# Optimization experiments

Measured on AMD Instinct MI355X. Metric: run time of the kernel, lower is better.

## Reference

```python
import jax, jax.numpy as jnp
import numpy as np

B, H, W, C = 4, 64, 64, 96
EXPAND = 2
D_INNER = EXPAND * C  # 192
N = 16   # d_state
K = 4    # scan directions
DT_RANK = int(np.ceil(C / 16))  # 6


def setup_inputs() -> dict:
    key = jax.random.key(0)
    ks = jax.random.split(key, 8)
    def rn(k, shape, scale=0.02):
        return jax.random.normal(k, shape, dtype=jnp.float32) * scale
    return {
        "x": jax.random.normal(ks[0], (B, H, W, C), dtype=jnp.float32),
        "ln_g": jnp.ones((C,), jnp.float32),
        "ln_b": jnp.zeros((C,), jnp.float32),
        "in_proj_w": rn(ks[1], (C, 2 * D_INNER)),
        "in_proj_b": jnp.zeros((2 * D_INNER,), jnp.float32),
        "conv_w": rn(ks[2], (D_INNER, 1, 3, 3), 0.1),
        "conv_b": jnp.zeros((D_INNER,), jnp.float32),
        "x_proj_w": rn(ks[3], (K, DT_RANK + 2 * N, D_INNER)),
        "dt_proj_w": rn(ks[4], (K, D_INNER, DT_RANK), 0.1),
        "dt_proj_b": rn(ks[5], (K, D_INNER), 0.1),
        "A_logs": jnp.log(jnp.tile(jnp.arange(1, N + 1, dtype=jnp.float32)[None, :], (K * D_INNER, 1))),
        "Ds": jnp.ones((K * D_INNER,), jnp.float32),
        "out_norm_g": jnp.ones((D_INNER,), jnp.float32),
        "out_norm_b": jnp.zeros((D_INNER,), jnp.float32),
        "out_proj_w": rn(ks[6], (D_INNER, C)),
        "out_proj_b": jnp.zeros((C,), jnp.float32),
    }


def _ln(x, g, b, eps):
    mu = x.mean(-1, keepdims=True)
    var = jnp.mean((x - mu) ** 2, axis=-1, keepdims=True)
    return (x - mu) * jax.lax.rsqrt(var + eps) * g + b


def _vss_forward(x, ln_g, ln_b, in_proj_w, in_proj_b, conv_w, conv_b,
                 x_proj_w, dt_proj_w, dt_proj_b, A_logs, Ds,
                 out_norm_g, out_norm_b, out_proj_w, out_proj_b):
    Bb, Hh, Ww, Cc = x.shape
    L = Hh * Ww
    d = D_INNER
    # ln_1 (eps=1e-6), then SS2D on channels-first layout
    xn = _ln(x, ln_g, ln_b, 1e-6)
    xz = jnp.einsum('bhwc,ce->bhwe', xn, in_proj_w) + in_proj_b
    xi, z = jnp.split(xz, 2, axis=-1)
    xi = xi.transpose(0, 3, 1, 2)  # (B, d, H, W)
    xi = jax.lax.conv_general_dilated(
        xi, conv_w, (1, 1), 'SAME', feature_group_count=d,
        dimension_numbers=('NCHW', 'OIHW', 'NCHW'))
    xi = jax.nn.silu(xi + conv_b[None, :, None, None])
    # 4 scan directions: row-major, col-major, and their reverses
    x_hw = xi.reshape(Bb, d, L)
    x_wh = xi.transpose(0, 1, 3, 2).reshape(Bb, d, L)
    xs = jnp.stack([x_hw, x_wh], axis=1)                      # (B,2,d,L)
    xs = jnp.concatenate([xs, jnp.flip(xs, axis=-1)], axis=1)  # (B,K,d,L)
    x_dbl = jnp.einsum('bkdl,kcd->bkcl', xs, x_proj_w)         # (B,K,R+2N,L)
    dt_r = x_dbl[:, :, :DT_RANK]
    Bs = x_dbl[:, :, DT_RANK:DT_RANK + N]                      # (B,K,N,L)
    Cs = x_dbl[:, :, DT_RANK + N:]                             # (B,K,N,L)
    dts = jnp.einsum('bkrl,kdr->bkdl', dt_r, dt_proj_w)
    dts = jax.nn.softplus(dts + dt_proj_b[None, :, :, None])
    A = -jnp.exp(A_logs).reshape(K, d, N)
    Dsk = Ds.reshape(K, d)

    def step(h, inp):
        u_t, dt_t, B_t, C_t = inp                  # (B,K,d),(B,K,d),(B,K,N),(B,K,N)
        dA = jnp.exp(dt_t[..., None] * A)          # (B,K,d,N)
        h = dA * h + (dt_t * u_t)[..., None] * B_t[:, :, None, :]
        y = jnp.einsum('bkdn,bkn->bkd', h, C_t)
        return h, y

    seq = (xs.transpose(3, 0, 1, 2), dts.transpose(3, 0, 1, 2),
           Bs.transpose(3, 0, 1, 2), Cs.transpose(3, 0, 1, 2))
    h0 = jnp.zeros((Bb, K, d, N), xs.dtype)
    _, ys = jax.lax.scan(step, h0, seq)            # ys: (L,B,K,d)
    ys = ys.transpose(1, 2, 3, 0)                  # (B,K,d,L)
    ys = ys + Dsk[None, :, :, None] * xs
    # merge the 4 directions back into one row-major map
    inv_y = jnp.flip(ys[:, 2:4], axis=-1)
    wh_y = ys[:, 1].reshape(Bb, d, Ww, Hh).transpose(0, 1, 3, 2).reshape(Bb, d, L)
    invwh_y = inv_y[:, 1].reshape(Bb, d, Ww, Hh).transpose(0, 1, 3, 2).reshape(Bb, d, L)
    y = ys[:, 0] + inv_y[:, 0] + wh_y + invwh_y    # (B,d,L)
    y = y.transpose(0, 2, 1).reshape(Bb, Hh, Ww, d)
    y = _ln(y, out_norm_g, out_norm_b, 1e-5)
    y = y * jax.nn.silu(z)
    out = jnp.einsum('bhwd,dc->bhwc', y, out_proj_w) + out_proj_b
    return x + out  # residual (drop_path = 0 -> identity)


def reference(x, ln_g, ln_b, in_proj_w, in_proj_b, conv_w, conv_b, x_proj_w,
              dt_proj_w, dt_proj_b, A_logs, Ds, out_norm_g, out_norm_b,
              out_proj_w, out_proj_b):
    return _vss_forward(x, ln_g, ln_b, in_proj_w, in_proj_b, conv_w, conv_b,
                        x_proj_w, dt_proj_w, dt_proj_b, A_logs, Ds,
                        out_norm_g, out_norm_b, out_proj_w, out_proj_b)
```

## Files before the change

kernel.cpp:

```cpp
#include <hip/hip_runtime.h>
#include <math.h>

#define CC   96
#define DIN  192
#define NST  16
#define KDIR 4
#define DTR  6
#define LL   4096
#define BB   4
#define NSEG 64
#define SEGLEN 64
#define XROW 40

#define NROW ((long)BB*LL)
#define SZ_BLD ((long)BB*LL*DIN)

__device__ __forceinline__ float sigmoidf_(float x){
    return __builtin_amdgcn_rcpf(1.0f + __expf(-x));
}
__device__ __forceinline__ int whmap(int l){ return ((l & 63) << 6) | (l >> 6); }
__device__ __forceinline__ int mapk(int k, int l){
    switch(k & 3){
        case 0:  return l;
        case 1:  return whmap(l);
        case 2:  return LL - 1 - l;
        default: return whmap(LL - 1 - l);
    }
}

__global__ __launch_bounds__(384) void kA(const float* __restrict__ x,
        const float* __restrict__ lng, const float* __restrict__ lnb,
        const float* __restrict__ W,   const float* __restrict__ bias,
        float* __restrict__ xi, float* __restrict__ z)
{
    __shared__ float xn[16*96];
    __shared__ float sc1[384], sc2[384];
    __shared__ float mu[16], rs[16];
    int t = threadIdx.x;
    long row0 = (long)blockIdx.x * 16;

    for(int q=t; q<16*96; q+=384) xn[q] = x[row0*96 + q];
    __syncthreads();

    {
        int r = t/24, i = t%24;
        float s=0.f, ss=0.f;
        #pragma unroll
        for(int j=0;j<4;j++){ float v = xn[r*96 + i + j*24]; s+=v; ss+=v*v; }
        sc1[t]=s; sc2[t]=ss;
        __syncthreads();
        if(t<16){
            float S=0.f, SS=0.f;
            for(int j=0;j<24;j++){ S+=sc1[t*24+j]; SS+=sc2[t*24+j]; }
            float m = S*(1.0f/96.0f);
            float var = SS*(1.0f/96.0f) - m*m;
            mu[t]=m; rs[t]=rsqrtf(var + 1e-6f);
        }
        __syncthreads();
    }
    for(int q=t; q<16*96; q+=384){
        int r=q/96, c=q%96;
        xn[q] = (xn[q]-mu[r])*rs[r]*lng[c] + lnb[c];
    }
    __syncthreads();

    float acc[16];
    #pragma unroll
    for(int r=0;r<16;r++) acc[r]=0.f;
    for(int c=0;c<96;c++){
        float wv = W[c*384 + t];
        #pragma unroll
        for(int r=0;r<16;r++) acc[r] = fmaf(xn[r*96+c], wv, acc[r]);
    }
    float bv = bias[t];
    if(t < 192){
        for(int r=0;r<16;r++) xi[(row0+r)*DIN + t] = acc[r] + bv;
    } else {
        int e = t - 192;
        for(int r=0;r<16;r++) z[(row0+r)*DIN + e] = acc[r] + bv;
    }
}

__global__ __launch_bounds__(256) void kB(const float* __restrict__ xi,
        const float* __restrict__ cw, const float* __restrict__ cb,
        float* __restrict__ xc)
{
    long idx = (long)blockIdx.x*256 + threadIdx.x;
    if(idx >= SZ_BLD) return;
    int d = (int)(idx % DIN);
    long rg = idx / DIN;
    int p = (int)(rg % LL); int b = (int)(rg / LL);
    int h = p >> 6, w = p & 63;
    float acc = 0.f;
    #pragma unroll
    for(int dh=0; dh<3; dh++){
        int hh = h + dh - 1;
        if(hh < 0 || hh >= 64) continue;
        #pragma unroll
        for(int dw=0; dw<3; dw++){
            int ww2 = w + dw - 1;
            if(ww2 < 0 || ww2 >= 64) continue;
            acc = fmaf(xi[((long)b*LL + hh*64 + ww2)*DIN + d], cw[d*9 + dh*3 + dw], acc);
        }
    }
    acc += cb[d];
    xc[idx] = acc * sigmoidf_(acc);
}

__global__ __launch_bounds__(192) void kC(const float* __restrict__ xc,
        const float* __restrict__ xw, float* __restrict__ xdbl)
{
    __shared__ float ls[16*192];
    int t = threadIdx.x;
    long row0 = (long)blockIdx.x * 16;
    int b  = (int)(row0 / LL);
    int p0 = (int)(row0 % LL);
    for(int q=t; q<16*192; q+=192) ls[q] = xc[row0*DIN + q];
    __syncthreads();
    if(t < 152){
        int k = t/38, c = t%38;
        const float* wr = xw + (long)(k*38 + c)*192;
        float acc[16];
        #pragma unroll
        for(int r=0;r<16;r++) acc[r]=0.f;
        for(int d=0; d<192; d+=4){
            float4 wv = *(const float4*)(wr + d);
            #pragma unroll
            for(int r=0;r<16;r++){
                float4 lv = *(const float4*)(&ls[r*192 + d]);
                acc[r] = fmaf(lv.x,wv.x, fmaf(lv.y,wv.y, fmaf(lv.z,wv.z, fmaf(lv.w,wv.w, acc[r]))));
            }
        }
        int cs = (c < 6) ? c : c + 2;
        for(int r=0;r<16;r++){
            int p = p0 + r;
            int lk;
            if(k==0) lk = p;
            else if(k==1) lk = whmap(p);
            else if(k==2) lk = LL-1-p;
            else lk = LL-1-whmap(p);
            xdbl[(((long)(b*KDIR + k)*LL + lk)*XROW) + cs] = acc[r];
        }
    }
}

__device__ __forceinline__ void dt_and_E(float s, float& dt, float& E){
    float eneg = __expf(-fabsf(s));
    dt = fmaxf(s, 0.f) + log1pf(eneg);
    float rcp = __builtin_amdgcn_rcpf(1.0f + eneg);
    E = (s > 0.f) ? eneg*rcp : rcp;
}
__device__ __forceinline__ void pow_tree(float E, float* En){
    En[0]=E;
    float E2=E*E;        En[1]=E2;
    En[2]=E2*E;  float E4=E2*E2; En[3]=E4;
    En[4]=E4*E;  En[5]=E4*E2;  En[6]=E4*En[2];
    float E8=E4*E4;      En[7]=E8;
    En[8]=E8*E;  En[9]=E8*E2;  En[10]=E8*En[2]; En[11]=E8*E4;
    En[12]=E8*En[4]; En[13]=E8*En[5]; En[14]=E8*En[6]; En[15]=E8*E8;
}

__global__ __launch_bounds__(192) void kD(const float* __restrict__ xc,
        const float* __restrict__ xdbl, const float* __restrict__ alog,
        const float* __restrict__ dtw,  const float* __restrict__ dtb,
        const float* __restrict__ Ds,
        float* __restrict__ ys0, float* __restrict__ ys123,
        float* __restrict__ hend, float* __restrict__ dtsum)
{
    __shared__ float rows[SEGLEN*XROW];
    int t = threadIdx.x;
    int blk = blockIdx.x;
    int bk = blk / NSEG, seg = blk % NSEG;
    int b = bk / KDIR, k = bk % KDIR;
    {
        const float* src = xdbl + ((long)bk*LL + seg*SEGLEN)*XROW;
        for(int q=t; q<SEGLEN*XROW; q+=192) rows[q] = src[q];
    }
    int d = t;
    int kd = k*192 + d;
    float a[16]; bool fast = true;
    #pragma unroll
    for(int n=0;n<16;n++){
        a[n] = -__expf(alog[kd*16 + n]);
        fast = fast && (fabsf(a[n] + (float)(n+1)) < 1e-3f);
    }
    float w6[6];
    #pragma unroll
    for(int r=0;r<6;r++) w6[r] = dtw[kd*6 + r];
    float bdt = dtb[kd];
    float Dd  = Ds[kd];
    float* ybuf = (k==0) ? ys0 : (ys123 + (long)(k-1)*SZ_BLD);
    float h[16];
    #pragma unroll
    for(int n=0;n<16;n++) h[n]=0.f;
    float sdt = 0.f;
    __syncthreads();

    int lg0 = seg * SEGLEN;
    int p = mapk(k, lg0);
    float u = xc[((long)b*LL + p)*DIN + d];
    for(int i=0; i<SEGLEN; i++){
        const float* row = &rows[i*XROW];
        float s = bdt;
        #pragma unroll
        for(int r=0;r<6;r++) s = fmaf(row[r], w6[r], s);
        float dt, E; dt_and_E(s, dt, E);
        sdt += dt;
        float wi = dt * u;
        int pn = 0; float unext = 0.f;
        if(i+1 < SEGLEN){
            pn = mapk(k, lg0 + i + 1);
            unext = xc[((long)b*LL + pn)*DIN + d];
        }
        float En[16];
        if(fast){ pow_tree(E, En); }
        else { 
            #pragma unroll
            for(int n=0;n<16;n++) En[n] = __expf(dt * a[n]);
        }
        float Bv[16], Cv[16];
        #pragma unroll
        for(int n=0;n<16;n+=4){
            *(float4*)(Bv+n) = *(const float4*)(row + 8 + n);
            *(float4*)(Cv+n) = *(const float4*)(row + 24 + n);
        }
        float y = Dd * u;
        #pragma unroll
        for(int n=0;n<16;n++){
            h[n] = fmaf(En[n], h[n], wi*Bv[n]);
            y = fmaf(h[n], Cv[n], y);
        }
        ybuf[((long)b*LL + p)*DIN + d] = y;
        p = pn; u = unext;
    }
    long hb = (((long)bk*NSEG + seg)*192 + d)*16;
    #pragma unroll
    for(int n=0;n<16;n+=4)
        *(float4*)(&hend[hb+n]) = make_float4(h[n],h[n+1],h[n+2],h[n+3]);
    dtsum[((long)bk*NSEG + seg)*192 + d] = sdt;
}

__global__ __launch_bounds__(256) void kE(const float* __restrict__ alog,
        const float* __restrict__ dtsum, float* __restrict__ hx)
{
    int tid = blockIdx.x*256 + threadIdx.x;
    int n = tid & 15;
    int d = (tid >> 4) % 192;
    int bk = tid / (192*16);
    int k = bk % KDIR;
    float an = -__expf(alog[(k*192 + d)*16 + n]);
    float H = 0.f;
    for(int seg=0; seg<NSEG; seg++){
        long base = ((long)bk*NSEG + seg)*3072 + d*16 + n;
        float he = hx[base];
        hx[base] = H;
        float P = __expf(an * dtsum[((long)bk*NSEG + seg)*192 + d]);
        H = fmaf(P, H, he);
    }
}

__global__ __launch_bounds__(192) void kF(const float* __restrict__ xdbl,
        const float* __restrict__ alog, const float* __restrict__ dtw,
        const float* __restrict__ dtb,  const float* __restrict__ Hprev,
        float* __restrict__ ys0, float* __restrict__ ys123)
{
    int blk = blockIdx.x;
    int bk = blk / NSEG, seg = blk % NSEG;
    if(seg == 0) return;
    __shared__ float rows[SEGLEN*XROW];
    int t = threadIdx.x;
    int b = bk / KDIR, k = bk % KDIR;
    {
        const float* src = xdbl + ((long)bk*LL + seg*SEGLEN)*XROW;
        for(int q=t; q<SEGLEN*XROW; q+=192) rows[q] = src[q];
    }
    int d = t;
    int kd = k*192 + d;
    float a[16]; bool fast = true;
    #pragma unroll
    for(int n=0;n<16;n++){
        a[n] = -__expf(alog[kd*16 + n]);
        fast = fast && (fabsf(a[n] + (float)(n+1)) < 1e-3f);
    }
    float w6[6];
    #pragma unroll
    for(int r=0;r<6;r++) w6[r] = dtw[kd*6 + r];
    float bdt = dtb[kd];
    float g[16];
    long hb = (((long)bk*NSEG + seg)*192 + d)*16;
    #pragma unroll
    for(int n=0;n<16;n+=4){
        float4 v = *(const float4*)(&Hprev[hb+n]);
        g[n]=v.x; g[n+1]=v.y; g[n+2]=v.z; g[n+3]=v.w;
    }
    float* ybuf = (k==0) ? ys0 : (ys123 + (long)(k-1)*SZ_BLD);
    __syncthreads();

    int lg0 = seg * SEGLEN;
    int p = mapk(k, lg0);
    for(int i=0; i<SEGLEN; i++){
        const float* row = &rows[i*XROW];
        float s = bdt;
        #pragma unroll
        for(int r=0;r<6;r++) s = fmaf(row[r], w6[r], s);
        float dt, E; dt_and_E(s, dt, E);
        float En[16];
        if(fast){ pow_tree(E, En); }
        else {
            #pragma unroll
            for(int n=0;n<16;n++) En[n] = __expf(dt * a[n]);
        }
        float Cv[16];
        #pragma unroll
        for(int n=0;n<16;n+=4) *(float4*)(Cv+n) = *(const float4*)(row + 24 + n);
        float yc = 0.f;
        #pragma unroll
        for(int n=0;n<16;n++){
            g[n] *= En[n];
            yc = fmaf(g[n], Cv[n], yc);
        }
        long addr = ((long)b*LL + p)*DIN + d;
        ybuf[addr] += yc;
        if(i+1 < SEGLEN) p = mapk(k, lg0 + i + 1);
    }
}

__global__ __launch_bounds__(384) void kG(const float* __restrict__ ys0,
        const float* __restrict__ ys123, const float* __restrict__ z,
        const float* __restrict__ ong, const float* __restrict__ onb,
        const float* __restrict__ Wout, const float* __restrict__ ob,
        const float* __restrict__ x, float* __restrict__ out)
{
    __shared__ float yb[16*192];
    __shared__ float sc1[384], sc2[384];
    __shared__ float mu[16], rs[16];
    int t = threadIdx.x;
    long row0 = (long)blockIdx.x * 16;

    for(int q=t; q<3072; q+=384){
        long off = row0*DIN + q;
        yb[q] = ys0[off] + ys123[off] + ys123[SZ_BLD + off] + ys123[2*SZ_BLD + off];
    }
    __syncthreads();
    {
        int r = t/24, i = t%24;
        float s=0.f, ss=0.f;
        #pragma unroll
        for(int j=0;j<8;j++){ float v = yb[r*192 + i*8 + j]; s+=v; ss+=v*v; }
        sc1[t]=s; sc2[t]=ss;
        __syncthreads();
        if(t<16){
            float S=0.f, SS=0.f;
            for(int j=0;j<24;j++){ S+=sc1[t*24+j]; SS+=sc2[t*24+j]; }
            float m = S*(1.0f/192.0f);
            float var = SS*(1.0f/192.0f) - m*m;
            mu[t]=m; rs[t]=rsqrtf(var + 1e-5f);
        }
        __syncthreads();
    }
    for(int q=t; q<3072; q+=384){
        int r=q/192, dd=q%192;
        float v = (yb[q]-mu[r])*rs[r]*ong[dd] + onb[dd];
        float zz = z[row0*DIN + q];
        yb[q] = v * (zz * sigmoidf_(zz));
    }
    __syncthreads();
    int c = t % 96, rg4 = t / 96;
    float acc[4] = {0.f,0.f,0.f,0.f};
    for(int dd=0; dd<192; dd++){
        float wv = Wout[dd*96 + c];
        #pragma unroll
        for(int j=0;j<4;j++) acc[j] = fmaf(yb[(rg4*4+j)*192 + dd], wv, acc[j]);
    }
    float bv = ob[c];
    for(int j=0;j<4;j++){
        long row = row0 + rg4*4 + j;
        out[row*96 + c] = x[row*96 + c] + acc[j] + bv;
    }
}

extern "C" void kernel_launch(void* const* d_in, const int* in_sizes, int n_in,
                              void* d_out, int out_size, void* d_ws, size_t ws_size,
                              hipStream_t stream)
{
    const float* x    = (const float*)d_in[0];
    const float* lng  = (const float*)d_in[1];
    const float* lnb  = (const float*)d_in[2];
    const float* ipw  = (const float*)d_in[3];
    const float* ipb  = (const float*)d_in[4];
    const float* cw   = (const float*)d_in[5];
    const float* cb   = (const float*)d_in[6];
    const float* xpw  = (const float*)d_in[7];
    const float* dtw  = (const float*)d_in[8];
    const float* dtb  = (const float*)d_in[9];
    const float* alog = (const float*)d_in[10];
    const float* Ds   = (const float*)d_in[11];
    const float* ong  = (const float*)d_in[12];
    const float* onb  = (const float*)d_in[13];
    const float* opw  = (const float*)d_in[14];
    const float* opb  = (const float*)d_in[15];

    float* ws    = (float*)d_ws;
    float* xi    = ws + 0;
    float* z     = ws + 3145728;
    float* xc    = ws + 6291456;
    float* xdbl  = ws + 9437184;
    float* ys123 = ws + 12058624;
    float* hx    = ws + 21495808;
    float* dtsum = ws + 24641536;
    float* ys0   = xi;
    float* out   = (float*)d_out;

    hipLaunchKernelGGL(kA, dim3(1024),  dim3(384), 0, stream, x, lng, lnb, ipw, ipb, xi, z);
    hipLaunchKernelGGL(kB, dim3(12288), dim3(256), 0, stream, xi, cw, cb, xc);
    hipLaunchKernelGGL(kC, dim3(1024),  dim3(192), 0, stream, xc, xpw, xdbl);
    hipLaunchKernelGGL(kD, dim3(1024),  dim3(192), 0, stream, xc, xdbl, alog, dtw, dtb, Ds,
                       ys0, ys123, hx, dtsum);
    hipLaunchKernelGGL(kE, dim3(192),   dim3(256), 0, stream, alog, dtsum, hx);
    hipLaunchKernelGGL(kF, dim3(1024),  dim3(192), 0, stream, xdbl, alog, dtw, dtb, hx,
                       ys0, ys123);
    hipLaunchKernelGGL(kG, dim3(1024),  dim3(384), 0, stream, ys0, ys123, z, ong, onb,
                       opw, opb, x, out);
}
```

Measured before the change: 343.1 us.

## Restructure chunked scan: state-only first pass, full recompute with carry-in second pass

The first scan pass now computes only the per-segment end states and dt sums, without producing outputs. The second pass starts from the propagated carry-in state and recomputes the full recurrence, so it writes final y directly instead of doing a read-modify-write correction. Segment length is halved to double the number of blocks. The carry-propagation kernel is reorganized to one block per (batch, direction) with prefetching, and softplus/exp use exp2/log intrinsics with strided address stepping. The cost is recomputing the recurrence in the second pass and the kE2 pass now being serial over 128 segments in only 16 blocks.

```diff
diff --git a/kernel.cpp b/kernel.cpp
--- a/kernel.cpp
+++ b/kernel.cpp
@@ -8,11 +8,10 @@
 #define DTR  6
 #define LL   4096
 #define BB   4
-#define NSEG 64
-#define SEGLEN 64
+#define NSEG 128
+#define SEGLEN 32
 #define XROW 40
 
-#define NROW ((long)BB*LL)
 #define SZ_BLD ((long)BB*LL*DIN)
 
 __device__ __forceinline__ float sigmoidf_(float x){
@@ -28,6 +27,34 @@
     }
 }
 
+__device__ __forceinline__ void dt_and_E(float s, float& dt, float& E){
+    const float LOG2E = 1.4426950408889634f;
+    const float LN2   = 0.6931471805599453f;
+    float sn  = s * LOG2E;
+    float t   = __builtin_amdgcn_exp2f(-fabsf(sn));
+    float opt = 1.0f + t;
+    float r   = __builtin_amdgcn_rcpf(opt);
+    E  = (s > 0.f) ? t*r : r;
+    dt = LN2 * (fmaxf(sn, 0.f) + __builtin_amdgcn_logf(opt));
+}
+__device__ __forceinline__ void pow_tree(float E, float* En){
+    En[0]=E;
+    float E2=E*E;        En[1]=E2;
+    En[2]=E2*E;  float E4=E2*E2; En[3]=E4;
+    En[4]=E4*E;  En[5]=E4*E2;  En[6]=E4*En[2];
+    float E8=E4*E4;      En[7]=E8;
+    En[8]=E8*E;  En[9]=E8*E2;  En[10]=E8*En[2]; En[11]=E8*E4;
+    En[12]=E8*En[4]; En[13]=E8*En[5]; En[14]=E8*En[6]; En[15]=E8*E8;
+}
+__device__ __forceinline__ void dir_base(int k, int lg0, int& p0, int& stride){
+    switch(k & 3){
+        case 0:  p0 = lg0;               stride = 1;   break;
+        case 1:  p0 = whmap(lg0);        stride = 64;  break;
+        case 2:  p0 = LL - 1 - lg0;      stride = -1;  break;
+        default: p0 = whmap(LL-1-lg0);   stride = -64; break;
+    }
+}
+
 __global__ __launch_bounds__(384) void kA(const float* __restrict__ x,
         const float* __restrict__ lng, const float* __restrict__ lnb,
         const float* __restrict__ W,   const float* __restrict__ bias,
@@ -41,7 +68,6 @@
 
     for(int q=t; q<16*96; q+=384) xn[q] = x[row0*96 + q];
     __syncthreads();
-
     {
         int r = t/24, i = t%24;
         float s=0.f, ss=0.f;
@@ -144,27 +170,9 @@
     }
 }
 
-__device__ __forceinline__ void dt_and_E(float s, float& dt, float& E){
-    float eneg = __expf(-fabsf(s));
-    dt = fmaxf(s, 0.f) + log1pf(eneg);
-    float rcp = __builtin_amdgcn_rcpf(1.0f + eneg);
-    E = (s > 0.f) ? eneg*rcp : rcp;
-}
-__device__ __forceinline__ void pow_tree(float E, float* En){
-    En[0]=E;
-    float E2=E*E;        En[1]=E2;
-    En[2]=E2*E;  float E4=E2*E2; En[3]=E4;
-    En[4]=E4*E;  En[5]=E4*E2;  En[6]=E4*En[2];
-    float E8=E4*E4;      En[7]=E8;
-    En[8]=E8*E;  En[9]=E8*E2;  En[10]=E8*En[2]; En[11]=E8*E4;
-    En[12]=E8*En[4]; En[13]=E8*En[5]; En[14]=E8*En[6]; En[15]=E8*E8;
-}
-
-__global__ __launch_bounds__(192) void kD(const float* __restrict__ xc,
+__global__ __launch_bounds__(192) void kD2(const float* __restrict__ xc,
         const float* __restrict__ xdbl, const float* __restrict__ alog,
         const float* __restrict__ dtw,  const float* __restrict__ dtb,
-        const float* __restrict__ Ds,
-        float* __restrict__ ys0, float* __restrict__ ys123,
         float* __restrict__ hend, float* __restrict__ dtsum)
 {
     __shared__ float rows[SEGLEN*XROW];
@@ -176,8 +184,7 @@
         const float* src = xdbl + ((long)bk*LL + seg*SEGLEN)*XROW;
         for(int q=t; q<SEGLEN*XROW; q+=192) rows[q] = src[q];
     }
-    int d = t;
-    int kd = k*192 + d;
+    int d = t, kd = k*192 + d;
     float a[16]; bool fast = true;
     #pragma unroll
     for(int n=0;n<16;n++){
@@ -188,17 +195,19 @@
     #pragma unroll
     for(int r=0;r<6;r++) w6[r] = dtw[kd*6 + r];
     float bdt = dtb[kd];
-    float Dd  = Ds[kd];
-    float* ybuf = (k==0) ? ys0 : (ys123 + (long)(k-1)*SZ_BLD);
+
+    int lg0 = seg * SEGLEN;
+    int p0, stride; dir_base(k, lg0, p0, stride);
+    long addr  = ((long)b*LL + p0)*DIN + d;
+    long astep = (long)stride*DIN;
+
     float h[16];
     #pragma unroll
     for(int n=0;n<16;n++) h[n]=0.f;
     float sdt = 0.f;
     __syncthreads();
 
-    int lg0 = seg * SEGLEN;
-    int p = mapk(k, lg0);
-    float u = xc[((long)b*LL + p)*DIN + d];
+    float u = xc[addr];
     for(int i=0; i<SEGLEN; i++){
         const float* row = &rows[i*XROW];
         float s = bdt;
@@ -207,121 +216,150 @@
         float dt, E; dt_and_E(s, dt, E);
         sdt += dt;
         float wi = dt * u;
-        int pn = 0; float unext = 0.f;
-        if(i+1 < SEGLEN){
-            pn = mapk(k, lg0 + i + 1);
-            unext = xc[((long)b*LL + pn)*DIN + d];
-        }
-        float En[16];
-        if(fast){ pow_tree(E, En); }
-        else { 
-            #pragma unroll
-            for(int n=0;n<16;n++) En[n] = __expf(dt * a[n]);
-        }
-        float Bv[16], Cv[16];
-        #pragma unroll
-        for(int n=0;n<16;n+=4){
-            *(float4*)(Bv+n) = *(const float4*)(row + 8 + n);
-            *(float4*)(Cv+n) = *(const float4*)(row + 24 + n);
-        }
-        float y = Dd * u;
-        #pragma unroll
-        for(int n=0;n<16;n++){
-            h[n] = fmaf(En[n], h[n], wi*Bv[n]);
-            y = fmaf(h[n], Cv[n], y);
-        }
-        ybuf[((long)b*LL + p)*DIN + d] = y;
-        p = pn; u = unext;
-    }
-    long hb = (((long)bk*NSEG + seg)*192 + d)*16;
-    #pragma unroll
-    for(int n=0;n<16;n+=4)
-        *(float4*)(&hend[hb+n]) = make_float4(h[n],h[n+1],h[n+2],h[n+3]);
-    dtsum[((long)bk*NSEG + seg)*192 + d] = sdt;
-}
-
-__global__ __launch_bounds__(256) void kE(const float* __restrict__ alog,
-        const float* __restrict__ dtsum, float* __restrict__ hx)
-{
-    int tid = blockIdx.x*256 + threadIdx.x;
-    int n = tid & 15;
-    int d = (tid >> 4) % 192;
-    int bk = tid / (192*16);
-    int k = bk % KDIR;
-    float an = -__expf(alog[(k*192 + d)*16 + n]);
-    float H = 0.f;
-    for(int seg=0; seg<NSEG; seg++){
-        long base = ((long)bk*NSEG + seg)*3072 + d*16 + n;
-        float he = hx[base];
-        hx[base] = H;
-        float P = __expf(an * dtsum[((long)bk*NSEG + seg)*192 + d]);
-        H = fmaf(P, H, he);
-    }
-}
-
-__global__ __launch_bounds__(192) void kF(const float* __restrict__ xdbl,
-        const float* __restrict__ alog, const float* __restrict__ dtw,
-        const float* __restrict__ dtb,  const float* __restrict__ Hprev,
-        float* __restrict__ ys0, float* __restrict__ ys123)
-{
-    int blk = blockIdx.x;
-    int bk = blk / NSEG, seg = blk % NSEG;
-    if(seg == 0) return;
-    __shared__ float rows[SEGLEN*XROW];
-    int t = threadIdx.x;
-    int b = bk / KDIR, k = bk % KDIR;
-    {
-        const float* src = xdbl + ((long)bk*LL + seg*SEGLEN)*XROW;
-        for(int q=t; q<SEGLEN*XROW; q+=192) rows[q] = src[q];
-    }
-    int d = t;
-    int kd = k*192 + d;
-    float a[16]; bool fast = true;
-    #pragma unroll
-    for(int n=0;n<16;n++){
-        a[n] = -__expf(alog[kd*16 + n]);
-        fast = fast && (fabsf(a[n] + (float)(n+1)) < 1e-3f);
-    }
-    float w6[6];
-    #pragma unroll
-    for(int r=0;r<6;r++) w6[r] = dtw[kd*6 + r];
-    float bdt = dtb[kd];
-    float g[16];
-    long hb = (((long)bk*NSEG + seg)*192 + d)*16;
-    #pragma unroll
-    for(int n=0;n<16;n+=4){
-        float4 v = *(const float4*)(&Hprev[hb+n]);
-        g[n]=v.x; g[n+1]=v.y; g[n+2]=v.z; g[n+3]=v.w;
-    }
-    float* ybuf = (k==0) ? ys0 : (ys123 + (long)(k-1)*SZ_BLD);
-    __syncthreads();
-
-    int lg0 = seg * SEGLEN;
-    int p = mapk(k, lg0);
-    for(int i=0; i<SEGLEN; i++){
-        const float* row = &rows[i*XROW];
-        float s = bdt;
-        #pragma unroll
-        for(int r=0;r<6;r++) s = fmaf(row[r], w6[r], s);
-        float dt, E; dt_and_E(s, dt, E);
+        float unext = 0.f;
+        long addrN = addr + astep;
+        if(i+1 < SEGLEN) unext = xc[addrN];
         float En[16];
         if(fast){ pow_tree(E, En); }
         else {
             #pragma unroll
             for(int n=0;n<16;n++) En[n] = __expf(dt * a[n]);
         }
-        float Cv[16];
-        #pragma unroll
-        for(int n=0;n<16;n+=4) *(float4*)(Cv+n) = *(const float4*)(row + 24 + n);
-        float yc = 0.f;
+        float Bv[16];
+        #pragma unroll
+        for(int n=0;n<16;n+=4) *(float4*)(Bv+n) = *(const float4*)(row + 8 + n);
+        #pragma unroll
+        for(int n=0;n<16;n++) h[n] = fmaf(En[n], h[n], wi*Bv[n]);
+        addr = addrN; u = unext;
+    }
+    long hb = (((long)bk*NSEG + seg)*192 + d)*16;
+    #pragma unroll
+    for(int n=0;n<16;n+=4)
+        *(float4*)(&hend[hb+n]) = make_float4(h[n],h[n+1],h[n+2],h[n+3]);
+    dtsum[((long)bk*NSEG + seg)*192 + d] = sdt;
+}
+
+__global__ __launch_bounds__(256) void kE2(const float* __restrict__ alog,
+        const float* __restrict__ dtsum, float* __restrict__ hx)
+{
+    int bk = blockIdx.x;
+    int k = bk & 3;
+    int t = threadIdx.x;
+    float an[12], H[12];
+    #pragma unroll
+    for(int j=0;j<12;j++){
+        int sidx = j*256 + t;
+        int d = sidx >> 4, n = sidx & 15;
+        an[j] = -__expf(alog[(k*192 + d)*16 + n]);
+        H[j] = 0.f;
+    }
+    long hbase = (long)bk*NSEG*3072;
+    long sbase = (long)bk*NSEG*192;
+    float he[12], sd[12];
+    #pragma unroll
+    for(int j=0;j<12;j++){
+        he[j] = hx[hbase + j*256 + t];
+        sd[j] = dtsum[sbase + ((j*256 + t) >> 4)];
+    }
+    for(int seg=0; seg<NSEG; seg++){
+        float heN[12], sdN[12];
+        if(seg+1 < NSEG){
+            long h2 = hbase + (long)(seg+1)*3072;
+            long s2 = sbase + (long)(seg+1)*192;
+            #pragma unroll
+            for(int j=0;j<12;j++){
+                heN[j] = hx[h2 + j*256 + t];
+                sdN[j] = dtsum[s2 + ((j*256 + t) >> 4)];
+            }
+        } else {
+            #pragma unroll
+            for(int j=0;j<12;j++){ heN[j]=0.f; sdN[j]=0.f; }
+        }
+        long h1 = hbase + (long)seg*3072;
+        #pragma unroll
+        for(int j=0;j<12;j++){
+            float P = __expf(an[j]*sd[j]);
+            hx[h1 + j*256 + t] = H[j];
+            H[j] = fmaf(P, H[j], he[j]);
+        }
+        #pragma unroll
+        for(int j=0;j<12;j++){ he[j]=heN[j]; sd[j]=sdN[j]; }
+    }
+}
+
+__global__ __launch_bounds__(192) void kF2(const float* __restrict__ xc,
+        const float* __restrict__ xdbl, const float* __restrict__ alog,
+        const float* __restrict__ dtw,  const float* __restrict__ dtb,
+        const float* __restrict__ Ds,   const float* __restrict__ Hprev,
+        float* __restrict__ ys0, float* __restrict__ ys123)
+{
+    __shared__ float rows[SEGLEN*XROW];
+    int t = threadIdx.x;
+    int blk = blockIdx.x;
+    int bk = blk / NSEG, seg = blk % NSEG;
+    int b = bk / KDIR, k = bk % KDIR;
+    {
+        const float* src = xdbl + ((long)bk*LL + seg*SEGLEN)*XROW;
+        for(int q=t; q<SEGLEN*XROW; q+=192) rows[q] = src[q];
+    }
+    int d = t, kd = k*192 + d;
+    float a[16]; bool fast = true;
+    #pragma unroll
+    for(int n=0;n<16;n++){
+        a[n] = -__expf(alog[kd*16 + n]);
+        fast = fast && (fabsf(a[n] + (float)(n+1)) < 1e-3f);
+    }
+    float w6[6];
+    #pragma unroll
+    for(int r=0;r<6;r++) w6[r] = dtw[kd*6 + r];
+    float bdt = dtb[kd];
+    float Dd  = Ds[kd];
+    float h[16];
+    long hb = (((long)bk*NSEG + seg)*192 + d)*16;
+    #pragma unroll
+    for(int n=0;n<16;n+=4){
+        float4 v = *(const float4*)(&Hprev[hb+n]);
+        h[n]=v.x; h[n+1]=v.y; h[n+2]=v.z; h[n+3]=v.w;
+    }
+    float* ybuf = (k==0) ? ys0 : (ys123 + (long)(k-1)*SZ_BLD);
+
+    int lg0 = seg * SEGLEN;
+    int p0, stride; dir_base(k, lg0, p0, stride);
+    long addr  = ((long)b*LL + p0)*DIN + d;
+    long astep = (long)stride*DIN;
+    __syncthreads();
+
+    float u = xc[addr];
+    for(int i=0; i<SEGLEN; i++){
+        const float* row = &rows[i*XROW];
+        float s = bdt;
+        #pragma unroll
+        for(int r=0;r<6;r++) s = fmaf(row[r], w6[r], s);
+        float dt, E; dt_and_E(s, dt, E);
+        float wi = dt * u;
+        float unext = 0.f;
+        long addrN = addr + astep;
+        if(i+1 < SEGLEN) unext = xc[addrN];
+        float En[16];
+        if(fast){ pow_tree(E, En); }
+        else {
+            #pragma unroll
+            for(int n=0;n<16;n++) En[n] = __expf(dt * a[n]);
+        }
+        float Bv[16], Cv[16];
+        #pragma unroll
+        for(int n=0;n<16;n+=4){
+            *(float4*)(Bv+n) = *(const float4*)(row + 8 + n);
+            *(float4*)(Cv+n) = *(const float4*)(row + 24 + n);
+        }
+        float y = Dd * u;
         #pragma unroll
         for(int n=0;n<16;n++){
-            g[n] *= En[n];
-            yc = fmaf(g[n], Cv[n], yc);
-        }
-        long addr = ((long)b*LL + p)*DIN + d;
-        ybuf[addr] += yc;
-        if(i+1 < SEGLEN) p = mapk(k, lg0 + i + 1);
+            h[n] = fmaf(En[n], h[n], wi*Bv[n]);
+            y = fmaf(h[n], Cv[n], y);
+        }
+        ybuf[addr] = y;
+        addr = addrN; u = unext;
     }
 }
 
@@ -407,18 +445,18 @@
     float* xdbl  = ws + 9437184;
     float* ys123 = ws + 12058624;
     float* hx    = ws + 21495808;
-    float* dtsum = ws + 24641536;
+    float* dtsum = ws + 27787264;
     float* ys0   = xi;
     float* out   = (float*)d_out;
 
-    hipLaunchKernelGGL(kA, dim3(1024),  dim3(384), 0, stream, x, lng, lnb, ipw, ipb, xi, z);
-    hipLaunchKernelGGL(kB, dim3(12288), dim3(256), 0, stream, xi, cw, cb, xc);
-    hipLaunchKernelGGL(kC, dim3(1024),  dim3(192), 0, stream, xc, xpw, xdbl);
-    hipLaunchKernelGGL(kD, dim3(1024),  dim3(192), 0, stream, xc, xdbl, alog, dtw, dtb, Ds,
-                       ys0, ys123, hx, dtsum);
-    hipLaunchKernelGGL(kE, dim3(192),   dim3(256), 0, stream, alog, dtsum, hx);
-    hipLaunchKernelGGL(kF, dim3(1024),  dim3(192), 0, stream, xdbl, alog, dtw, dtb, hx,
-                       ys0, ys123);
-    hipLaunchKernelGGL(kG, dim3(1024),  dim3(384), 0, stream, ys0, ys123, z, ong, onb,
+    hipLaunchKernelGGL(kA,  dim3(1024),  dim3(384), 0, stream, x, lng, lnb, ipw, ipb, xi, z);
+    hipLaunchKernelGGL(kB,  dim3(12288), dim3(256), 0, stream, xi, cw, cb, xc);
+    hipLaunchKernelGGL(kC,  dim3(1024),  dim3(192), 0, stream, xc, xpw, xdbl);
+    hipLaunchKernelGGL(kD2, dim3(2048),  dim3(192), 0, stream, xc, xdbl, alog, dtw, dtb,
+                       hx, dtsum);
+    hipLaunchKernelGGL(kE2, dim3(16),    dim3(256), 0, stream, alog, dtsum, hx);
+    hipLaunchKernelGGL(kF2, dim3(2048),  dim3(192), 0, stream, xc, xdbl, alog, dtw, dtb,
+                       Ds, hx, ys0, ys123);
+    hipLaunchKernelGGL(kG,  dim3(1024),  dim3(384), 0, stream, ys0, ys123, z, ong, onb,
                        opw, opb, x, out);
 }
```

Result: slower. 351.2 us (+2.4%).
